# Performance work log

Hardware: AMD Instinct MI355X
Metric: run time of the kernel (lower is better)

The kernel has to match this reference:

```python
import jax, jax.numpy as jnp
import numpy as np

B, C, H, W = 16, 384, 56, 56
NH, WS, SS = 12, 7, 3          # num_heads, window_size, shift_size
MLP = 4 * C
N = WS * WS                     # tokens per window (49)
nHW = H // WS                   # windows per side (8)
nW = nHW * nHW                  # windows per image (64)
HD = C // NH                    # head dim (32)
EPS = 1e-5


def _ln(x, g, b):
    mu = jnp.mean(x, axis=-1, keepdims=True)
    var = jnp.mean(jnp.square(x - mu), axis=-1, keepdims=True)
    return (x - mu) * jax.lax.rsqrt(var + EPS) * g + b


def _attn_mask():
    # static shifted-window mask, computed once with numpy (constants)
    img = np.zeros((H, W))
    sl = (slice(0, -WS), slice(-WS, -SS), slice(-SS, None))
    cnt = 0
    for hs in sl:
        for ws_ in sl:
            img[hs, ws_] = cnt
            cnt += 1
    mw = img.reshape(nHW, WS, nHW, WS).transpose(0, 2, 1, 3).reshape(-1, N)
    d = mw[:, None, :] - mw[:, :, None]          # (nW, N, N)
    return jnp.asarray(np.where(d != 0, -100.0, 0.0), jnp.float32)

_MASK = _attn_mask()


def setup_inputs() -> dict:
    key = jax.random.key(0)
    ks = jax.random.split(key, 6)
    rn = lambda k, s: jax.random.normal(k, s, jnp.float32) * 0.02
    return {
        "x": jax.random.normal(ks[0], (B, C, H, W), jnp.float32),
        "norm1_g": jnp.ones((C,), jnp.float32),
        "norm1_b": jnp.zeros((C,), jnp.float32),
        "qkv_w": rn(ks[1], (C, 3 * C)),
        "qkv_b": jnp.zeros((3 * C,), jnp.float32),
        "proj_w": rn(ks[2], (C, C)),
        "proj_b": jnp.zeros((C,), jnp.float32),
        "norm2_g": jnp.ones((C,), jnp.float32),
        "norm2_b": jnp.zeros((C,), jnp.float32),
        "fc1_w": rn(ks[3], (C, MLP)),
        "fc1_b": jnp.zeros((MLP,), jnp.float32),
        "fc2_w": rn(ks[4], (MLP, C)),
        "fc2_b": jnp.zeros((C,), jnp.float32),
    }


def reference(x, norm1_g, norm1_b, qkv_w, qkv_b, proj_w, proj_b,
              norm2_g, norm2_b, fc1_w, fc1_b, fc2_w, fc2_b):
    shortcut = x                                   # (B, C, H, W)
    xh = jnp.transpose(x, (0, 2, 3, 1))            # (B, H, W, C)
    xh = _ln(xh, norm1_g, norm1_b)
    # H, W divisible by WS -> padding is a no-op; shifted window path
    xs = jnp.roll(xh, (-SS, -SS), axis=(1, 2))
    # window partition -> (B*nW, N, C)
    xw = xs.reshape(B, nHW, WS, nHW, WS, C).transpose(0, 1, 3, 2, 4, 5)
    xw = xw.reshape(-1, N, C)
    # attention
    qkv = (xw @ qkv_w + qkv_b).reshape(-1, N, 3, NH, HD).transpose(2, 0, 3, 1, 4)
    q, k, v = qkv[0] * HD ** -0.5, qkv[1], qkv[2]  # (B*nW, NH, N, HD)
    attn = jnp.einsum('whnd,whmd->whnm', q, k)     # (B*nW, NH, N, N)
    attn = attn.reshape(B, nW, NH, N, N) + _MASK[None, :, None]
    attn = jax.nn.softmax(attn, axis=-1).reshape(-1, NH, N, N)
    out = jnp.einsum('whnm,whmd->whnd', attn, v)   # (B*nW, NH, N, HD)
    out = out.transpose(0, 2, 1, 3).reshape(-1, N, C)
    out = out @ proj_w + proj_b
    # window reverse -> (B, H, W, C), un-shift
    xs = out.reshape(B, nHW, nHW, WS, WS, C).transpose(0, 1, 3, 2, 4, 5)
    xs = xs.reshape(B, H, W, C)
    xh = jnp.roll(xs, (SS, SS), axis=(1, 2))
    x2 = shortcut + jnp.transpose(xh, (0, 3, 1, 2))
    # MLP residual (in BHWC)
    xh2 = jnp.transpose(x2, (0, 2, 3, 1))
    h = jax.nn.gelu(_ln(xh2, norm2_g, norm2_b) @ fc1_w + fc1_b,
                    approximate=False) @ fc2_w + fc2_b
    xh2 = xh2 + h
    return jnp.transpose(xh2, (0, 3, 1, 2))
```

## Files before the change

### kernel.cpp

```cpp
#include <hip/hip_runtime.h>
#include <hip/hip_bf16.h>
#include <math.h>
#include <stdint.h>

#define C_ 384
#define TOKENS 50176

typedef __bf16 bf16;
typedef __bf16 bf16x8 __attribute__((ext_vector_type(8)));
typedef float  f32x4  __attribute__((ext_vector_type(4)));

__device__ __forceinline__ float b2f(bf16 x) { return (float)x; }
__device__ __forceinline__ bf16  f2b(float x) { return (bf16)x; }

__device__ __forceinline__ void gld_lds16(const bf16* g, bf16* l) {
    __builtin_amdgcn_global_load_lds(
        (const __attribute__((address_space(1))) void*)g,
        (__attribute__((address_space(3))) void*)l, 16, 0, 0);
}

__global__ void wtrans_kernel(const float* __restrict__ in, bf16* __restrict__ out,
                              int K, int N) {
    int idx = blockIdx.x * 256 + threadIdx.x;
    if (idx >= K * N) return;
    int n = idx / K, k = idx % K;
    out[idx] = f2b(in[(size_t)k * N + n]);
}

__global__ __launch_bounds__(256) void ln1_gather_kernel(
    const float* __restrict__ x, const float* __restrict__ g,
    const float* __restrict__ bt, bf16* __restrict__ xw) {
    int wave = threadIdx.x >> 6, lane = threadIdx.x & 63;
    int T = blockIdx.x * 4 + wave;
    int wi = T / 49, n = T % 49;
    int b = wi >> 6, w64 = wi & 63;
    int bh = w64 >> 3, bw = w64 & 7;
    int hs = bh * 7 + n / 7 + 3; if (hs >= 56) hs -= 56;
    int wsd = bw * 7 + n % 7 + 3; if (wsd >= 56) wsd -= 56;
    const float* xp = x + (size_t)b * C_ * 3136 + hs * 56 + wsd;
    float v[6];
    #pragma unroll
    for (int k = 0; k < 6; k++) v[k] = xp[(size_t)(lane + k * 64) * 3136];
    float s = v[0] + v[1] + v[2] + v[3] + v[4] + v[5];
    #pragma unroll
    for (int m = 32; m; m >>= 1) s += __shfl_xor(s, m);
    float mu = s * (1.0f / 384.0f);
    float s2 = 0.f;
    #pragma unroll
    for (int k = 0; k < 6; k++) { float d = v[k] - mu; s2 += d * d; }
    #pragma unroll
    for (int m = 32; m; m >>= 1) s2 += __shfl_xor(s2, m);
    float rstd = rsqrtf(s2 * (1.0f / 384.0f) + 1e-5f);
    bf16* op = xw + (size_t)T * 384;
    #pragma unroll
    for (int k = 0; k < 6; k++) {
        int c = lane + k * 64;
        op[c] = f2b((v[k] - mu) * rstd * g[c] + bt[c]);
    }
}

enum { EPI_NONE = 0, EPI_GELU = 1, EPI_PROJ = 2, EPI_FC2 = 3 };

template <int EPI>
__global__ __launch_bounds__(256) void gemm_kernel(
    const bf16* __restrict__ A, const bf16* __restrict__ Wt,
    const float* __restrict__ bias, bf16* __restrict__ Cout,
    int Kdim, int Ndim,
    const float* __restrict__ resx,
    const bf16* __restrict__ resb) {
    __shared__ __align__(16) bf16 As[128 * 32];
    __shared__ __align__(16) bf16 Bs[128 * 32];
    int t = threadIdx.x;
    int m0 = blockIdx.x * 128, n0 = blockIdx.y * 128;
    int lane = t & 63, wave = t >> 6;
    int wr = wave >> 1, wc = wave & 1;
    int quad = lane >> 4, lm = lane & 15;
    f32x4 acc[4][4] = {};

    int c1 = t, c2 = t + 256;
    const bf16* ga1 = A + (size_t)(m0 + (c1 >> 2)) * Kdim + (c1 & 3) * 8;
    const bf16* ga2 = A + (size_t)(m0 + (c2 >> 2)) * Kdim + (c2 & 3) * 8;
    const bf16* gb1 = Wt + (size_t)(n0 + (c1 >> 2)) * Kdim + (c1 & 3) * 8;
    const bf16* gb2 = Wt + (size_t)(n0 + (c2 >> 2)) * Kdim + (c2 & 3) * 8;
    bf16* la1 = As + c1 * 8; bf16* la2 = As + c2 * 8;
    bf16* lb1 = Bs + c1 * 8; bf16* lb2 = Bs + c2 * 8;

    for (int k0 = 0; k0 < Kdim; k0 += 32) {
        gld_lds16(ga1 + k0, la1);
        gld_lds16(ga2 + k0, la2);
        gld_lds16(gb1 + k0, lb1);
        gld_lds16(gb2 + k0, lb2);
        __syncthreads();
        bf16x8 af[4], bfr[4];
        #pragma unroll
        for (int i = 0; i < 4; i++)
            af[i] = *(const bf16x8*)(As + (wr * 64 + i * 16 + lm) * 32 + quad * 8);
        #pragma unroll
        for (int j = 0; j < 4; j++)
            bfr[j] = *(const bf16x8*)(Bs + (wc * 64 + j * 16 + lm) * 32 + quad * 8);
        #pragma unroll
        for (int i = 0; i < 4; i++)
            #pragma unroll
            for (int j = 0; j < 4; j++)
                acc[i][j] = __builtin_amdgcn_mfma_f32_16x16x32_bf16(af[i], bfr[j], acc[i][j], 0, 0, 0);
        __syncthreads();
    }

    int col[4]; float bv[4];
    #pragma unroll
    for (int j = 0; j < 4; j++) { col[j] = n0 + wc * 64 + j * 16 + lm; bv[j] = bias[col[j]]; }
    #pragma unroll
    for (int i = 0; i < 4; i++) {
        #pragma unroll
        for (int r = 0; r < 4; r++) {
            int row = m0 + wr * 64 + i * 16 + quad * 4 + r;
            size_t resbase = 0;
            if (EPI == EPI_PROJ) {
                int wi = row / 49, n = row % 49;
                int b = wi >> 6, w64 = wi & 63;
                int bh = w64 >> 3, bw = w64 & 7;
                int hs = bh * 7 + n / 7 + 3; if (hs >= 56) hs -= 56;
                int wsd = bw * 7 + n % 7 + 3; if (wsd >= 56) wsd -= 56;
                resbase = (size_t)b * C_ * 3136 + hs * 56 + wsd;
            }
            #pragma unroll
            for (int j = 0; j < 4; j++) {
                float v = acc[i][j][r] + bv[j];
                if (EPI == EPI_GELU) v = 0.5f * v * (1.0f + erff(v * 0.70710678118f));
                if (EPI == EPI_PROJ) v += resx[resbase + (size_t)col[j] * 3136];
                if (EPI == EPI_FC2)  v += b2f(resb[(size_t)row * 384 + col[j]]);
                Cout[(size_t)row * Ndim + col[j]] = f2b(v);
            }
        }
    }
}

__global__ __launch_bounds__(64) void attn_mfma_kernel(const bf16* __restrict__ qkv,
                                                       bf16* __restrict__ aout) {
    __shared__ __align__(16) bf16 pbuf[64 * 72];
    __shared__ int reg_[64];
    int l = threadIdx.x;
    int wi = blockIdx.x / 12, h = blockIdx.x % 12;
    int i16 = l & 15, quad = l >> 4;

    {
        int tok = l < 49 ? l : 48;
        int w64 = wi & 63;
        int bh = w64 >> 3, bw = w64 & 7;
        int hh = bh * 7 + tok / 7, ww = bw * 7 + tok % 7;
        int fh = hh < 49 ? 0 : (hh < 53 ? 1 : 2);
        int fw = ww < 49 ? 0 : (ww < 53 ? 1 : 2);
        reg_[l] = fh * 3 + fw;
    }
    __syncthreads();

    const bf16* qbase = qkv + (size_t)wi * 49 * 1152 + h * 32;

    f32x4 s_[4][4] = {};
    bf16x8 af[4], bfr[4];
    #pragma unroll
    for (int mi = 0; mi < 4; mi++) {
        int m = mi * 16 + i16; if (m > 48) m = 48;
        af[mi] = *(const bf16x8*)(qbase + (size_t)m * 1152 + quad * 8);
    }
    #pragma unroll
    for (int nt = 0; nt < 4; nt++) {
        int n = nt * 16 + i16; if (n > 48) n = 48;
        bfr[nt] = *(const bf16x8*)(qbase + 384 + (size_t)n * 1152 + quad * 8);
    }
    #pragma unroll
    for (int mi = 0; mi < 4; mi++)
        #pragma unroll
        for (int nt = 0; nt < 4; nt++)
            s_[mi][nt] = __builtin_amdgcn_mfma_f32_16x16x32_bf16(af[mi], bfr[nt], s_[mi][nt], 0, 0, 0);

    int creg[4];
    #pragma unroll
    for (int nt = 0; nt < 4; nt++) {
        int c = nt * 16 + i16; if (c > 48) c = 48;
        creg[nt] = reg_[c];
    }

    const float scale = 0.17677669529663687f;
    #pragma unroll
    for (int mi = 0; mi < 4; mi++) {
        #pragma unroll
        for (int r = 0; r < 4; r++) {
            int row = mi * 16 + quad * 4 + r;
            int rreg = reg_[row];
            float v[4]; float mx = -1e30f;
            #pragma unroll
            for (int nt = 0; nt < 4; nt++) {
                int c = nt * 16 + i16;
                float x = s_[mi][nt][r] * scale;
                if (c > 48) x = -1e30f;
                else if (rreg != creg[nt]) x -= 100.0f;
                v[nt] = x; mx = fmaxf(mx, x);
            }
            #pragma unroll
            for (int m = 8; m; m >>= 1) mx = fmaxf(mx, __shfl_xor(mx, m));
            float sum = 0.f;
            #pragma unroll
            for (int nt = 0; nt < 4; nt++) { v[nt] = __expf(v[nt] - mx); sum += v[nt]; }
            #pragma unroll
            for (int m = 8; m; m >>= 1) sum += __shfl_xor(sum, m);
            float inv = 1.0f / sum;
            #pragma unroll
            for (int nt = 0; nt < 4; nt++)
                pbuf[row * 72 + nt * 16 + i16] = f2b(v[nt] * inv);
        }
    }
    __syncthreads();

    f32x4 o_[4][2] = {};
    const bf16* vbase = qkv + (size_t)wi * 49 * 1152 + 768 + h * 32;
    #pragma unroll
    for (int ks = 0; ks < 2; ks++) {
        bf16x8 pa[4];
        #pragma unroll
        for (int mi = 0; mi < 4; mi++)
            pa[mi] = *(const bf16x8*)(pbuf + (mi * 16 + i16) * 72 + ks * 32 + quad * 8);
        bf16x8 vb[2];
        #pragma unroll
        for (int nt = 0; nt < 2; nt++)
            #pragma unroll
            for (int j = 0; j < 8; j++) {
                int tok = ks * 32 + quad * 8 + j; if (tok > 48) tok = 48;
                vb[nt][j] = vbase[(size_t)tok * 1152 + nt * 16 + i16];
            }
        #pragma unroll
        for (int mi = 0; mi < 4; mi++)
            #pragma unroll
            for (int nt = 0; nt < 2; nt++)
                o_[mi][nt] = __builtin_amdgcn_mfma_f32_16x16x32_bf16(pa[mi], vb[nt], o_[mi][nt], 0, 0, 0);
    }

    bf16* obase = aout + (size_t)wi * 49 * 384 + h * 32;
    #pragma unroll
    for (int mi = 0; mi < 4; mi++)
        #pragma unroll
        for (int r = 0; r < 4; r++) {
            int row = mi * 16 + quad * 4 + r;
            if (row < 49) {
                #pragma unroll
                for (int nt = 0; nt < 2; nt++)
                    obase[(size_t)row * 384 + nt * 16 + i16] = f2b(o_[mi][nt][r]);
            }
        }
}

__global__ __launch_bounds__(256) void ln2_kernel(const bf16* __restrict__ x2,
                                                  const float* __restrict__ g,
                                                  const float* __restrict__ bt,
                                                  bf16* __restrict__ x2n) {
    int wave = threadIdx.x >> 6, lane = threadIdx.x & 63;
    int T = blockIdx.x * 4 + wave;
    const bf16* xp = x2 + (size_t)T * 384;
    float v[6];
    #pragma unroll
    for (int k = 0; k < 6; k++) v[k] = b2f(xp[lane + k * 64]);
    float s = v[0] + v[1] + v[2] + v[3] + v[4] + v[5];
    #pragma unroll
    for (int m = 32; m; m >>= 1) s += __shfl_xor(s, m);
    float mu = s * (1.0f / 384.0f);
    float s2 = 0.f;
    #pragma unroll
    for (int k = 0; k < 6; k++) { float d = v[k] - mu; s2 += d * d; }
    #pragma unroll
    for (int m = 32; m; m >>= 1) s2 += __shfl_xor(s2, m);
    float rstd = rsqrtf(s2 * (1.0f / 384.0f) + 1e-5f);
    bf16* op = x2n + (size_t)T * 384;
    #pragma unroll
    for (int k = 0; k < 6; k++) {
        int c = lane + k * 64;
        op[c] = f2b((v[k] - mu) * rstd * g[c] + bt[c]);
    }
}

__global__ __launch_bounds__(256) void untile_kernel(const bf16* __restrict__ otok,
                                                     float* __restrict__ out) {
    __shared__ float tile[56 * 65];
    int t = threadIdx.x;
    int b = blockIdx.x / 336;
    int rem = blockIdx.x % 336;
    int h = rem / 6;
    int c0 = (rem % 6) * 64;
    int hs = h + 53; if (hs >= 56) hs -= 56;
    int bh = hs / 7, th = hs % 7;
    #pragma unroll
    for (int pass = 0; pass < 14; pass++) {
        int w = pass * 4 + (t >> 6);
        int c = t & 63;
        int wsd = w + 53; if (wsd >= 56) wsd -= 56;
        int T = (b * 64 + bh * 8 + wsd / 7) * 49 + th * 7 + wsd % 7;
        tile[w * 65 + c] = b2f(otok[(size_t)T * 384 + c0 + c]);
    }
    __syncthreads();
    #pragma unroll
    for (int pass = 0; pass < 14; pass++) {
        int idx = pass * 256 + t;
        int c = idx / 56, w = idx % 56;
        out[((size_t)(b * 384 + c0 + c)) * 3136 + h * 56 + w] = tile[w * 65 + c];
    }
}

extern "C" void kernel_launch(void* const* d_in, const int* in_sizes, int n_in,
                              void* d_out, int out_size, void* d_ws, size_t ws_size,
                              hipStream_t stream) {
    (void)in_sizes; (void)n_in; (void)out_size; (void)ws_size;
    const float* x      = (const float*)d_in[0];
    const float* n1g    = (const float*)d_in[1];
    const float* n1b    = (const float*)d_in[2];
    const float* qkv_w  = (const float*)d_in[3];
    const float* qkv_b  = (const float*)d_in[4];
    const float* proj_w = (const float*)d_in[5];
    const float* proj_b = (const float*)d_in[6];
    const float* n2g    = (const float*)d_in[7];
    const float* n2b    = (const float*)d_in[8];
    const float* fc1_w  = (const float*)d_in[9];
    const float* fc1_b  = (const float*)d_in[10];
    const float* fc2_w  = (const float*)d_in[11];
    const float* fc2_b  = (const float*)d_in[12];
    float* out = (float*)d_out;
    char* ws = (char*)d_ws;

    bf16* qkv_wT = (bf16*)(ws + 0);
    bf16* proj_wT = (bf16*)(ws + 884736);
    bf16* fc1_wT = (bf16*)(ws + 1179648);
    bf16* fc2_wT = (bf16*)(ws + 2359296);
    bf16* xw   = (bf16*)(ws + 4194304);
    bf16* qkvb = (bf16*)(ws + 42729472);
    bf16* attn = (bf16*)(ws + 158334976);
    bf16* x2   = (bf16*)(ws + 4194304);
    bf16* x2n  = (bf16*)(ws + 42729472);
    bf16* h1   = (bf16*)(ws + 81264640);
    bf16* otok = (bf16*)(ws + 235405312);

    wtrans_kernel<<<(384 * 1152 + 255) / 256, 256, 0, stream>>>(qkv_w, qkv_wT, 384, 1152);
    wtrans_kernel<<<(384 * 384 + 255) / 256, 256, 0, stream>>>(proj_w, proj_wT, 384, 384);
    wtrans_kernel<<<(384 * 1536 + 255) / 256, 256, 0, stream>>>(fc1_w, fc1_wT, 384, 1536);
    wtrans_kernel<<<(1536 * 384 + 255) / 256, 256, 0, stream>>>(fc2_w, fc2_wT, 1536, 384);

    ln1_gather_kernel<<<TOKENS / 4, 256, 0, stream>>>(x, n1g, n1b, xw);

    gemm_kernel<EPI_NONE><<<dim3(392, 9), 256, 0, stream>>>(
        xw, qkv_wT, qkv_b, qkvb, 384, 1152, nullptr, nullptr);

    attn_mfma_kernel<<<12288, 64, 0, stream>>>(qkvb, attn);

    gemm_kernel<EPI_PROJ><<<dim3(392, 3), 256, 0, stream>>>(
        attn, proj_wT, proj_b, x2, 384, 384, x, nullptr);

    ln2_kernel<<<TOKENS / 4, 256, 0, stream>>>(x2, n2g, n2b, x2n);

    gemm_kernel<EPI_GELU><<<dim3(392, 12), 256, 0, stream>>>(
        x2n, fc1_wT, fc1_b, h1, 384, 1536, nullptr, nullptr);

    gemm_kernel<EPI_FC2><<<dim3(392, 3), 256, 0, stream>>>(
        h1, fc2_wT, fc2_b, otok, 1536, 384, nullptr, x2);

    untile_kernel<<<16 * 336, 256, 0, stream>>>(otok, out);
}
```

Before: 748.0 us.

## Restructure GEMM to stage full-K A strip in LDS and stream weights from global

The GEMM kernel now loads a 64-row by 384-wide slab of A into padded LDS once per K chunk and reads the B (weight) fragments directly from global/L2 into registers, instead of double-synchronised 32-wide K tiles for both operands. M-tile shrinks to 64 with compile-time K/N, launch bounds request 3 blocks per CU, and the grid doubles in x. The exact erf GELU is replaced with a tanh-style approximation via __expf, which changes numerics slightly. The aim is fewer barriers and better occupancy, at the cost of uncached-through-LDS weight loads and higher LDS footprint.

```diff
diff --git a/kernel.cpp b/kernel.cpp
--- a/kernel.cpp
+++ b/kernel.cpp
@@ -12,12 +12,6 @@
 
 __device__ __forceinline__ float b2f(bf16 x) { return (float)x; }
 __device__ __forceinline__ bf16  f2b(float x) { return (bf16)x; }
-
-__device__ __forceinline__ void gld_lds16(const bf16* g, bf16* l) {
-    __builtin_amdgcn_global_load_lds(
-        (const __attribute__((address_space(1))) void*)g,
-        (__attribute__((address_space(3))) void*)l, 16, 0, 0);
-}
 
 __global__ void wtrans_kernel(const float* __restrict__ in, bf16* __restrict__ out,
                               int K, int N) {
@@ -61,59 +55,61 @@
 
 enum { EPI_NONE = 0, EPI_GELU = 1, EPI_PROJ = 2, EPI_FC2 = 3 };
 
-template <int EPI>
-__global__ __launch_bounds__(256) void gemm_kernel(
+template <int EPI, int KD, int ND>
+__global__ __launch_bounds__(256, 3) void gemm_kernel(
     const bf16* __restrict__ A, const bf16* __restrict__ Wt,
     const float* __restrict__ bias, bf16* __restrict__ Cout,
-    int Kdim, int Ndim,
     const float* __restrict__ resx,
     const bf16* __restrict__ resb) {
-    __shared__ __align__(16) bf16 As[128 * 32];
-    __shared__ __align__(16) bf16 Bs[128 * 32];
+    __shared__ __align__(16) bf16 As[64 * 392];
     int t = threadIdx.x;
-    int m0 = blockIdx.x * 128, n0 = blockIdx.y * 128;
+    int m0 = blockIdx.x * 64, n0 = blockIdx.y * 128;
     int lane = t & 63, wave = t >> 6;
     int wr = wave >> 1, wc = wave & 1;
-    int quad = lane >> 4, lm = lane & 15;
-    f32x4 acc[4][4] = {};
-
-    int c1 = t, c2 = t + 256;
-    const bf16* ga1 = A + (size_t)(m0 + (c1 >> 2)) * Kdim + (c1 & 3) * 8;
-    const bf16* ga2 = A + (size_t)(m0 + (c2 >> 2)) * Kdim + (c2 & 3) * 8;
-    const bf16* gb1 = Wt + (size_t)(n0 + (c1 >> 2)) * Kdim + (c1 & 3) * 8;
-    const bf16* gb2 = Wt + (size_t)(n0 + (c2 >> 2)) * Kdim + (c2 & 3) * 8;
-    bf16* la1 = As + c1 * 8; bf16* la2 = As + c2 * 8;
-    bf16* lb1 = Bs + c1 * 8; bf16* lb2 = Bs + c2 * 8;
-
-    for (int k0 = 0; k0 < Kdim; k0 += 32) {
-        gld_lds16(ga1 + k0, la1);
-        gld_lds16(ga2 + k0, la2);
-        gld_lds16(gb1 + k0, lb1);
-        gld_lds16(gb2 + k0, lb2);
+    int quad = lane >> 4, i16 = lane & 15;
+    f32x4 acc[2][4] = {};
+
+    const int NCHUNK = KD / 384;
+    #pragma unroll
+    for (int kc = 0; kc < NCHUNK; kc++) {
+        if (NCHUNK > 1 && kc) __syncthreads();
+        {
+            const bf16* gA = A + (size_t)m0 * KD + kc * 384;
+            #pragma unroll
+            for (int j = 0; j < 12; j++) {
+                int u = t + 256 * j;
+                int row = u / 48, kq = u % 48;
+                bf16x8 val = *(const bf16x8*)(gA + (size_t)row * KD + kq * 8);
+                *(bf16x8*)(As + row * 392 + kq * 8) = val;
+            }
+        }
         __syncthreads();
-        bf16x8 af[4], bfr[4];
-        #pragma unroll
-        for (int i = 0; i < 4; i++)
-            af[i] = *(const bf16x8*)(As + (wr * 64 + i * 16 + lm) * 32 + quad * 8);
-        #pragma unroll
-        for (int j = 0; j < 4; j++)
-            bfr[j] = *(const bf16x8*)(Bs + (wc * 64 + j * 16 + lm) * 32 + quad * 8);
-        #pragma unroll
-        for (int i = 0; i < 4; i++)
-            #pragma unroll
-            for (int j = 0; j < 4; j++)
-                acc[i][j] = __builtin_amdgcn_mfma_f32_16x16x32_bf16(af[i], bfr[j], acc[i][j], 0, 0, 0);
-        __syncthreads();
+        const bf16* gB = Wt + (size_t)(n0 + wc * 64) * KD + kc * 384;
+        #pragma unroll
+        for (int ks = 0; ks < 12; ks++) {
+            bf16x8 af[2], bq[4];
+            #pragma unroll
+            for (int mi = 0; mi < 2; mi++)
+                af[mi] = *(const bf16x8*)(As + (wr * 32 + mi * 16 + i16) * 392 + ks * 32 + quad * 8);
+            #pragma unroll
+            for (int nt = 0; nt < 4; nt++)
+                bq[nt] = *(const bf16x8*)(gB + (size_t)(nt * 16 + i16) * KD + ks * 32 + quad * 8);
+            #pragma unroll
+            for (int mi = 0; mi < 2; mi++)
+                #pragma unroll
+                for (int nt = 0; nt < 4; nt++)
+                    acc[mi][nt] = __builtin_amdgcn_mfma_f32_16x16x32_bf16(af[mi], bq[nt], acc[mi][nt], 0, 0, 0);
+        }
     }
 
     int col[4]; float bv[4];
     #pragma unroll
-    for (int j = 0; j < 4; j++) { col[j] = n0 + wc * 64 + j * 16 + lm; bv[j] = bias[col[j]]; }
-    #pragma unroll
-    for (int i = 0; i < 4; i++) {
+    for (int nt = 0; nt < 4; nt++) { col[nt] = n0 + wc * 64 + nt * 16 + i16; bv[nt] = bias[col[nt]]; }
+    #pragma unroll
+    for (int mi = 0; mi < 2; mi++) {
         #pragma unroll
         for (int r = 0; r < 4; r++) {
-            int row = m0 + wr * 64 + i * 16 + quad * 4 + r;
+            int row = m0 + wr * 32 + mi * 16 + quad * 4 + r;
             size_t resbase = 0;
             if (EPI == EPI_PROJ) {
                 int wi = row / 49, n = row % 49;
@@ -124,12 +120,15 @@
                 resbase = (size_t)b * C_ * 3136 + hs * 56 + wsd;
             }
             #pragma unroll
-            for (int j = 0; j < 4; j++) {
-                float v = acc[i][j][r] + bv[j];
-                if (EPI == EPI_GELU) v = 0.5f * v * (1.0f + erff(v * 0.70710678118f));
-                if (EPI == EPI_PROJ) v += resx[resbase + (size_t)col[j] * 3136];
-                if (EPI == EPI_FC2)  v += b2f(resb[(size_t)row * 384 + col[j]]);
-                Cout[(size_t)row * Ndim + col[j]] = f2b(v);
+            for (int nt = 0; nt < 4; nt++) {
+                float v = acc[mi][nt][r] + bv[nt];
+                if (EPI == EPI_GELU) {
+                    float u = v * (0.79788456f + 0.035677408f * v * v);
+                    v = v / (1.0f + __expf(-2.0f * u));
+                }
+                if (EPI == EPI_PROJ) v += resx[resbase + (size_t)col[nt] * 3136];
+                if (EPI == EPI_FC2)  v += b2f(resb[(size_t)row * 384 + col[nt]]);
+                Cout[(size_t)row * ND + col[nt]] = f2b(v);
             }
         }
     }
@@ -343,21 +342,21 @@
 
     ln1_gather_kernel<<<TOKENS / 4, 256, 0, stream>>>(x, n1g, n1b, xw);
 
-    gemm_kernel<EPI_NONE><<<dim3(392, 9), 256, 0, stream>>>(
-        xw, qkv_wT, qkv_b, qkvb, 384, 1152, nullptr, nullptr);
+    gemm_kernel<EPI_NONE, 384, 1152><<<dim3(784, 9), 256, 0, stream>>>(
+        xw, qkv_wT, qkv_b, qkvb, nullptr, nullptr);
 
     attn_mfma_kernel<<<12288, 64, 0, stream>>>(qkvb, attn);
 
-    gemm_kernel<EPI_PROJ><<<dim3(392, 3), 256, 0, stream>>>(
-        attn, proj_wT, proj_b, x2, 384, 384, x, nullptr);
+    gemm_kernel<EPI_PROJ, 384, 384><<<dim3(784, 3), 256, 0, stream>>>(
+        attn, proj_wT, proj_b, x2, x, nullptr);
 
     ln2_kernel<<<TOKENS / 4, 256, 0, stream>>>(x2, n2g, n2b, x2n);
 
-    gemm_kernel<EPI_GELU><<<dim3(392, 12), 256, 0, stream>>>(
-        x2n, fc1_wT, fc1_b, h1, 384, 1536, nullptr, nullptr);
-
-    gemm_kernel<EPI_FC2><<<dim3(392, 3), 256, 0, stream>>>(
-        h1, fc2_wT, fc2_b, otok, 1536, 384, nullptr, x2);
+    gemm_kernel<EPI_GELU, 384, 1536><<<dim3(784, 12), 256, 0, stream>>>(
+        x2n, fc1_wT, fc1_b, h1, nullptr, nullptr);
+
+    gemm_kernel<EPI_FC2, 1536, 384><<<dim3(784, 3), 256, 0, stream>>>(
+        h1, fc2_wT, fc2_b, otok, nullptr, x2);
 
     untile_kernel<<<16 * 336, 256, 0, stream>>>(otok, out);
 }
```

Result: slower. 1.090 ms (+45.8%).
